# Performance work log

Hardware: AMD Instinct MI355X
Metric: run time of the kernel (lower is better)

## Reference

```python
import jax, jax.numpy as jnp
import numpy as np

D = 1024
H = 16
DH = D // H
MAX_TYPES = 256
B, L = 8, 1024
EPS = 1e-5


def setup_inputs() -> dict:
    key = jax.random.key(0)
    ks = jax.random.split(key, 16)
    s = 0.02
    return {
        'type_ids': jax.random.randint(ks[0], (B, L), 0, MAX_TYPES),
        'values': jax.random.normal(ks[1], (B, L, 1), jnp.float32),
        'deltas': jax.random.uniform(ks[2], (B, L, 1), jnp.float32),
        'type_emb': jax.random.normal(ks[3], (MAX_TYPES, D), jnp.float32) * s,
        'Wv': jax.random.normal(ks[4], (D, 1), jnp.float32) * s,
        'bv': jnp.zeros((D,), jnp.float32),
        'Wt': jax.random.normal(ks[5], (D, 1), jnp.float32) * s,
        'bt': jnp.zeros((D,), jnp.float32),
        'Win': jax.random.normal(ks[6], (3 * D, D), jnp.float32) * s,
        'bin': jnp.zeros((3 * D,), jnp.float32),
        'Wout': jax.random.normal(ks[7], (D, D), jnp.float32) * s,
        'bout': jnp.zeros((D,), jnp.float32),
        'W1': jax.random.normal(ks[8], (D, D), jnp.float32) * s,
        'b1': jnp.zeros((D,), jnp.float32),
        'W2': jax.random.normal(ks[9], (D, D), jnp.float32) * s,
        'b2': jnp.zeros((D,), jnp.float32),
        'gamma': jnp.ones((D,), jnp.float32),
        'beta': jnp.zeros((D,), jnp.float32),
    }


def _ln(x, gamma, beta):
    mu = jnp.mean(x, axis=-1, keepdims=True)
    var = jnp.mean(jnp.square(x - mu), axis=-1, keepdims=True)
    return (x - mu) * jax.lax.rsqrt(var + EPS) * gamma + beta


def reference(type_ids, values, deltas, type_emb, Wv, bv, Wt, bt,
              Win, bin, Wout, bout, W1, b1, W2, b2, gamma, beta):
    # fused embedding: type lookup + value/time linear projections
    h = type_emb[type_ids] + values @ Wv.T + bv + deltas @ Wt.T + bt  # [B,L,D]
    b, l, d = h.shape
    # multi-head self-attention (explicit weights path, need_weights=True)
    qkv = h @ Win.T + bin  # [B,L,3D]
    q, k, v = jnp.split(qkv, 3, axis=-1)
    q = q.reshape(b, l, H, DH)
    k = k.reshape(b, l, H, DH)
    v = v.reshape(b, l, H, DH)
    scale = 1.0 / jnp.sqrt(jnp.asarray(DH, h.dtype))
    scores = jnp.einsum('blhd,bmhd->bhlm', q, k) * scale  # [B,H,L,L]
    w = jax.nn.softmax(scores, axis=-1)
    attn = jnp.einsum('bhlm,bmhd->blhd', w, v).reshape(b, l, d)
    attn_out = attn @ Wout.T + bout
    h2 = _ln(h + attn_out, gamma, beta)
    ff = jax.nn.relu(h2 @ W1.T + b1) @ W2.T + b2
    h3 = _ln(h2 + ff, gamma, beta)
    pooled = h3.mean(axis=1)  # [B,D]
    attn_tokens = w.mean(axis=1).mean(axis=2)  # mean over heads, then keys -> [B,L]
    return pooled, attn_tokens
```

## Files before the change

kernel.cpp:

```cpp
#include <hip/hip_runtime.h>
#include <hip/hip_bf16.h>


#define Dm 1024
#define Hh 16
#define Bb 8
#define Ll 1024
#define Mm 8192
#define LNEPS 1e-5f

typedef __attribute__((ext_vector_type(8))) short s16x8;
typedef __attribute__((ext_vector_type(4))) short s16x4;
typedef __attribute__((ext_vector_type(4))) float f32x4;

using bf16 = __hip_bfloat16;

__device__ __forceinline__ short f2bs(float f) {
  return __builtin_bit_cast(short, __float2bfloat16(f));
}

__device__ __forceinline__ unsigned cvtpk(float lo, float hi) {
  unsigned r;
  asm("v_cvt_pk_bf16_f32 %0, %1, %2" : "=v"(r) : "v"(lo), "v"(hi));
  return r;
}

__device__ __forceinline__ void gload16(const void* g, void* l) {
  __builtin_amdgcn_global_load_lds(
      (__attribute__((address_space(1))) void*)g,
      (__attribute__((address_space(3))) void*)l, 16, 0, 0);
}

__global__ __launch_bounds__(256) void k_f2b(const float* __restrict__ x, bf16* __restrict__ y)
{
  const size_t i = ((size_t)blockIdx.x * 256 + threadIdx.x) * 4;
  const float4 v = *(const float4*)&x[i];
  s16x4 o;
  o[0] = f2bs(v.x); o[1] = f2bs(v.y); o[2] = f2bs(v.z); o[3] = f2bs(v.w);
  *(s16x4*)&y[i] = o;
}

__global__ __launch_bounds__(256) void k_embed(
    const int* __restrict__ tids, const float* __restrict__ vals, const float* __restrict__ dels,
    const float* __restrict__ temb, const float* __restrict__ Wv, const float* __restrict__ bv,
    const float* __restrict__ Wt, const float* __restrict__ bt,
    float* __restrict__ hf, bf16* __restrict__ hb)
{
  const int row = blockIdx.x;
  const int ty = tids[row];
  const float v = vals[row], dl = dels[row];
  const int d0 = threadIdx.x * 4;
  const float4 e  = *(const float4*)&temb[(size_t)ty * Dm + d0];
  const float4 wv = *(const float4*)&Wv[d0];
  const float4 c1 = *(const float4*)&bv[d0];
  const float4 wt = *(const float4*)&Wt[d0];
  const float4 c2 = *(const float4*)&bt[d0];
  float4 h;
  h.x = e.x + v * wv.x + c1.x + dl * wt.x + c2.x;
  h.y = e.y + v * wv.y + c1.y + dl * wt.y + c2.y;
  h.z = e.z + v * wv.z + c1.z + dl * wt.z + c2.z;
  h.w = e.w + v * wv.w + c1.w + dl * wt.w + c2.w;
  *(float4*)&hf[(size_t)row * Dm + d0] = h;
  s16x4 o;
  o[0] = f2bs(h.x); o[1] = f2bs(h.y); o[2] = f2bs(h.z); o[3] = f2bs(h.w);
  *(s16x4*)((short*)hb + (size_t)row * Dm + d0) = o;
}

template<bool RELU, bool OUTF, bool OUTB, bool RES>
__global__ __launch_bounds__(512) void k_gemm8(
    const bf16* __restrict__ A, const bf16* __restrict__ Bt,
    const float* __restrict__ bias, const float* __restrict__ res,
    float* __restrict__ outF, bf16* __restrict__ outB, const int N, const int K)
{
  __shared__ __attribute__((aligned(16))) short lds[49152];
  const int tid = threadIdx.x, lane = tid & 63, wave = tid >> 6;
  const int wr = wave >> 2, wc = wave & 3;
  const int l15 = lane & 15, lg = (lane >> 4) & 3;
  const int bm = blockIdx.x, bn = blockIdx.y;
  const int NT = K >> 6;

  const int rl = tid >> 3;
  const int swz = ((tid & 7) ^ (rl & 7)) * 8;
  const bf16* aSrc = A  + (size_t)(bm * 128 + rl) * K + swz;
  const bf16* bSrc = Bt + (size_t)(bn * 256 + rl) * K + swz;

  f32x4 acc[4][4] = {};

  auto stageA = [&](int t, int h) {
    gload16(aSrc + (size_t)h * 64 * K + t * 64,
            &lds[(t & 1) * 24576 + h * 4096 + tid * 8]);
  };
  auto stageB = [&](int t, int h) {
    gload16(bSrc + (size_t)h * 128 * K + t * 64,
            &lds[(t & 1) * 24576 + 8192 + h * 8192 + tid * 8]);
    gload16(bSrc + (size_t)(h * 128 + 64) * K + t * 64,
            &lds[(t & 1) * 24576 + 8192 + h * 8192 + 4096 + tid * 8]);
  };

  stageA(0, 0); stageA(0, 1); stageB(0, 0); stageB(0, 1);
  if (NT > 1) { stageA(1, 0); stageA(1, 1); }
  asm volatile("s_waitcnt vmcnt(2)" ::: "memory");
  __builtin_amdgcn_sched_barrier(0);
  __builtin_amdgcn_s_barrier();

  for (int t = 0; t < NT; ++t) {
    const int cb = (t & 1) * 24576;
    s16x8 fa[4][2], fb[2][2];

#pragma unroll
    for (int m = 0; m < 4; ++m)
#pragma unroll
      for (int ks = 0; ks < 2; ++ks) {
        const int row = wr * 64 + m * 16 + l15;
        fa[m][ks] = *(const s16x8*)&lds[cb + row * 64 + (((ks * 4 + lg) ^ (row & 7)) << 3)];
      }
#pragma unroll
    for (int n = 0; n < 2; ++n)
#pragma unroll
      for (int ks = 0; ks < 2; ++ks) {
        const int row = wc * 64 + n * 16 + l15;
        fb[n][ks] = *(const s16x8*)&lds[cb + 8192 + row * 64 + (((ks * 4 + lg) ^ (row & 7)) << 3)];
      }
    if (t + 1 < NT) { stageB(t + 1, 0); stageB(t + 1, 1); }
    __builtin_amdgcn_s_barrier();
    asm volatile("s_waitcnt lgkmcnt(0)" ::: "memory");
    __builtin_amdgcn_sched_barrier(0);
    __builtin_amdgcn_s_setprio(1);
#pragma unroll
    for (int m = 0; m < 4; ++m)
#pragma unroll
      for (int n = 0; n < 2; ++n)
#pragma unroll
        for (int ks = 0; ks < 2; ++ks)
          acc[m][n] = __builtin_amdgcn_mfma_f32_16x16x32_bf16(fa[m][ks], fb[n][ks], acc[m][n], 0, 0, 0);
    __builtin_amdgcn_s_setprio(0);
    __builtin_amdgcn_s_barrier();

#pragma unroll
    for (int n = 0; n < 2; ++n)
#pragma unroll
      for (int ks = 0; ks < 2; ++ks) {
        const int row = wc * 64 + (2 + n) * 16 + l15;
        fb[n][ks] = *(const s16x8*)&lds[cb + 8192 + row * 64 + (((ks * 4 + lg) ^ (row & 7)) << 3)];
      }
    if (t + 2 < NT) { stageA(t + 2, 0); stageA(t + 2, 1); }
    __builtin_amdgcn_s_barrier();
    asm volatile("s_waitcnt lgkmcnt(0)" ::: "memory");
    __builtin_amdgcn_sched_barrier(0);
    __builtin_amdgcn_s_setprio(1);
#pragma unroll
    for (int m = 0; m < 4; ++m)
#pragma unroll
      for (int n = 0; n < 2; ++n)
#pragma unroll
        for (int ks = 0; ks < 2; ++ks)
          acc[m][2 + n] = __builtin_amdgcn_mfma_f32_16x16x32_bf16(fa[m][ks], fb[n][ks], acc[m][2 + n], 0, 0, 0);
    __builtin_amdgcn_s_setprio(0);

    if (t + 1 < NT) {
      if (t + 2 < NT) asm volatile("s_waitcnt vmcnt(2)" ::: "memory");
      else            asm volatile("s_waitcnt vmcnt(0)" ::: "memory");
      __builtin_amdgcn_sched_barrier(0);
      __builtin_amdgcn_s_barrier();
    }
  }

#pragma unroll
  for (int n = 0; n < 4; ++n) {
    const int col = bn * 256 + wc * 64 + n * 16 + l15;
    const float bc = bias[col];
#pragma unroll
    for (int m = 0; m < 4; ++m) {
#pragma unroll
      for (int i = 0; i < 4; ++i) {
        const size_t row = (size_t)bm * 128 + wr * 64 + m * 16 + lg * 4 + i;
        float v = acc[m][n][i] + bc;
        if constexpr (RES)  v += res[row * N + col];
        if constexpr (RELU) v = fmaxf(v, 0.f);
        if constexpr (OUTF) outF[row * N + col] = v;
        if constexpr (OUTB) outB[row * N + col] = __float2bfloat16(v);
      }
    }
  }
}

__global__ __launch_bounds__(256) void k_vt(const bf16* __restrict__ qkv, bf16* __restrict__ vt)
{
  const int bh = blockIdx.x, lc = blockIdx.y;
  const int b = bh >> 4, h = bh & 15;
  __shared__ short tile[64][72];
  const int r = threadIdx.x >> 2;
  const int c0 = (threadIdx.x & 3) << 4;
  const short* src = (const short*)qkv + ((size_t)(b * Ll + lc * 64 + r)) * 3072 + 2048 + h * 64 + c0;
  const s16x8 x0 = *(const s16x8*)src;
  const s16x8 x1 = *(const s16x8*)(src + 8);
#pragma unroll
  for (int j = 0; j < 8; ++j) { tile[r][c0 + j] = x0[j]; tile[r][c0 + 8 + j] = x1[j]; }
  __syncthreads();
  s16x8 y0, y1;
#pragma unroll
  for (int j = 0; j < 8; ++j) { y0[j] = tile[c0 + j][r]; y1[j] = tile[c0 + 8 + j][r]; }
  short* dst = (short*)vt + ((size_t)(bh * 64 + r)) * Ll + lc * 64 + c0;
  *(s16x8*)dst = y0;
  *(s16x8*)(dst + 8) = y1;
}

__global__ __launch_bounds__(256) void k_attn(
    const bf16* __restrict__ qkv, const bf16* __restrict__ vt, bf16* __restrict__ attnb)
{
  const int bh = blockIdx.x;
  const int qb = blockIdx.y;
  const int b = bh >> 4, h = bh & 15;
  __shared__ __attribute__((aligned(16))) short lK[4096];
  __shared__ __attribute__((aligned(16))) short lV[4096];
  __shared__ __attribute__((aligned(16))) short lP[8192];
  const int tid = threadIdx.x, lane = tid & 63, wave = tid >> 6;
  const int l15 = lane & 15, lg = lane >> 4;
  const int qrow = wave * 32;
  const int l7 = l15 & 7;

  s16x8 qf[2][2];
#pragma unroll
  for (int mq = 0; mq < 2; ++mq)
#pragma unroll
    for (int ks = 0; ks < 2; ++ks)
      qf[mq][ks] = *(const s16x8*)((const short*)qkv +
          ((size_t)(b * Ll + qb * 128 + qrow + mq * 16 + l15)) * 3072 + h * 64 + ks * 32 + lg * 8);

  f32x4 o[2][4] = {};
  float rs[2] = {0.f, 0.f};

  const int sr = tid >> 3;
  const int swz = (tid & 7) ^ (sr & 7);

  for (int mc = 0; mc < 16; ++mc) {
    __syncthreads();
    {
      const bf16* gk = qkv + ((size_t)(b * Ll + mc * 64 + sr)) * 3072 + 1024 + h * 64 + swz * 8;
      gload16(gk,                     &lK[tid * 8]);
      gload16(gk + (size_t)32 * 3072, &lK[2048 + tid * 8]);
      const bf16* gv = vt + ((size_t)(bh * 64 + sr)) * Ll + mc * 64 + swz * 8;
      gload16(gv,                   &lV[tid * 8]);
      gload16(gv + (size_t)32 * Ll, &lV[2048 + tid * 8]);
    }
    __syncthreads();

    f32x4 st[2][4] = {};
    __builtin_amdgcn_s_setprio(1);
#pragma unroll
    for (int ks = 0; ks < 2; ++ks) {
#pragma unroll
      for (int n = 0; n < 4; ++n) {
        const int kr = n * 16 + l15;
        const s16x8 kf = *(const s16x8*)&lK[kr * 64 + (((ks * 4 + lg) ^ l7) << 3)];
        st[0][n] = __builtin_amdgcn_mfma_f32_16x16x32_bf16(kf, qf[0][ks], st[0][n], 0, 0, 0);
        st[1][n] = __builtin_amdgcn_mfma_f32_16x16x32_bf16(kf, qf[1][ks], st[1][n], 0, 0, 0);
      }
    }
    __builtin_amdgcn_s_setprio(0);

#pragma unroll
    for (int mq = 0; mq < 2; ++mq) {
      const int qr = qrow + mq * 16 + l15;
      short* prow = &lP[qr * 64];
      float loc = 0.f;
#pragma unroll
      for (int n = 0; n < 4; ++n) {
        const float e0 = __expf(st[mq][n][0] * 0.125f);
        const float e1 = __expf(st[mq][n][1] * 0.125f);
        const float e2 = __expf(st[mq][n][2] * 0.125f);
        const float e3 = __expf(st[mq][n][3] * 0.125f);
        loc += (e0 + e1) + (e2 + e3);
        const unsigned c0 = cvtpk(e0, e1);
        const unsigned c1 = cvtpk(e2, e3);
        const int col0 = n * 16 + lg * 4;
        const int scol = ((((col0 >> 3) ^ (qr & 7)) << 3) | (col0 & 7));
        *(unsigned*)&prow[scol]     = c0;
        *(unsigned*)&prow[scol + 2] = c1;
      }
      rs[mq] += loc;
    }

    __builtin_amdgcn_s_setprio(1);
#pragma unroll
    for (int ks = 0; ks < 2; ++ks) {
      s16x8 pa[2];
#pragma unroll
      for (int mq = 0; mq < 2; ++mq) {
        const int qr = qrow + mq * 16 + l15;
        pa[mq] = *(const s16x8*)&lP[qr * 64 + (((ks * 4 + lg) ^ (qr & 7)) << 3)];
      }
#pragma unroll
      for (int dn = 0; dn < 4; ++dn) {
        const int vr = dn * 16 + l15;
        const s16x8 vf = *(const s16x8*)&lV[vr * 64 + (((ks * 4 + lg) ^ l7) << 3)];
        o[0][dn] = __builtin_amdgcn_mfma_f32_16x16x32_bf16(pa[0], vf, o[0][dn], 0, 0, 0);
        o[1][dn] = __builtin_amdgcn_mfma_f32_16x16x32_bf16(pa[1], vf, o[1][dn], 0, 0, 0);
      }
    }
    __builtin_amdgcn_s_setprio(0);
  }

#pragma unroll
  for (int mq = 0; mq < 2; ++mq) {
    rs[mq] += __shfl_xor(rs[mq], 16);
    rs[mq] += __shfl_xor(rs[mq], 32);
  }
#pragma unroll
  for (int mq = 0; mq < 2; ++mq) {
    float inv[4];
#pragma unroll
    for (int i = 0; i < 4; ++i)
      inv[i] = 1.f / __shfl(rs[mq], lg * 4 + i);
#pragma unroll
    for (int dn = 0; dn < 4; ++dn) {
#pragma unroll
      for (int i = 0; i < 4; ++i) {
        const int q = qb * 128 + qrow + mq * 16 + lg * 4 + i;
        attnb[((size_t)(b * Ll + q)) * Dm + h * 64 + dn * 16 + l15] =
            __float2bfloat16(o[mq][dn][i] * inv[i]);
      }
    }
  }
}

template<bool WB>
__global__ __launch_bounds__(256) void k_ln(const float* __restrict__ x,
    const float* __restrict__ gamma, const float* __restrict__ beta,
    float* __restrict__ yf, bf16* __restrict__ yb)
{
  const size_t row = blockIdx.x;
  const int d0 = threadIdx.x * 4;
  const float4 xv = *(const float4*)&x[row * Dm + d0];
  float s  = xv.x + xv.y + xv.z + xv.w;
  float ss = xv.x * xv.x + xv.y * xv.y + xv.z * xv.z + xv.w * xv.w;
#pragma unroll
  for (int m = 1; m < 64; m <<= 1) { s += __shfl_xor(s, m); ss += __shfl_xor(ss, m); }
  __shared__ float red[8];
  const int wv = threadIdx.x >> 6;
  if ((threadIdx.x & 63) == 0) { red[wv] = s; red[4 + wv] = ss; }
  __syncthreads();
  s  = red[0] + red[1] + red[2] + red[3];
  ss = red[4] + red[5] + red[6] + red[7];
  const float mu = s * (1.f / Dm);
  const float rstd = rsqrtf(ss * (1.f / Dm) - mu * mu + LNEPS);
  const float4 g  = *(const float4*)&gamma[d0];
  const float4 be = *(const float4*)&beta[d0];
  float4 y;
  y.x = (xv.x - mu) * rstd * g.x + be.x;
  y.y = (xv.y - mu) * rstd * g.y + be.y;
  y.z = (xv.z - mu) * rstd * g.z + be.z;
  y.w = (xv.w - mu) * rstd * g.w + be.w;
  *(float4*)&yf[row * Dm + d0] = y;
  if constexpr (WB) {
    s16x4 o;
    o[0] = f2bs(y.x); o[1] = f2bs(y.y); o[2] = f2bs(y.z); o[3] = f2bs(y.w);
    *(s16x4*)((short*)yb + row * Dm + d0) = o;
  }
}

__global__ __launch_bounds__(256) void k_pool_part(const float* __restrict__ h3, float* __restrict__ part)
{
  const int b = blockIdx.x, lcn = blockIdx.y, dz = blockIdx.z;
  const int d = dz * 256 + threadIdx.x;
  float s = 0.f;
#pragma unroll 4
  for (int l = 0; l < 64; ++l)
    s += h3[((size_t)(b * Ll + lcn * 64 + l)) * Dm + d];
  part[((size_t)(b * 16 + lcn)) * Dm + d] = s;
}

__global__ __launch_bounds__(256) void k_pool_fin(const float* __restrict__ part, float* __restrict__ out)
{
  const int b = blockIdx.x;
  const int d = blockIdx.y * 256 + threadIdx.x;
  float s = 0.f;
#pragma unroll
  for (int c = 0; c < 16; ++c) s += part[((size_t)(b * 16 + c)) * Dm + d];
  out[b * Dm + d] = s * (1.f / Ll);
  out[(size_t)Mm + b * Dm + d] = 1.f / Ll;
}

extern "C" void kernel_launch(void* const* d_in, const int* in_sizes, int n_in,
                              void* d_out, int out_size, void* d_ws, size_t ws_size,
                              hipStream_t stream) {
  const int*   tids  = (const int*)  d_in[0];
  const float* vals  = (const float*)d_in[1];
  const float* dels  = (const float*)d_in[2];
  const float* temb  = (const float*)d_in[3];
  const float* Wv    = (const float*)d_in[4];
  const float* bv    = (const float*)d_in[5];
  const float* Wt    = (const float*)d_in[6];
  const float* bt    = (const float*)d_in[7];
  const float* Win   = (const float*)d_in[8];
  const float* bin   = (const float*)d_in[9];
  const float* Wout  = (const float*)d_in[10];
  const float* bout  = (const float*)d_in[11];
  const float* W1    = (const float*)d_in[12];
  const float* b1    = (const float*)d_in[13];
  const float* W2    = (const float*)d_in[14];
  const float* b2    = (const float*)d_in[15];
  const float* gamma = (const float*)d_in[16];
  const float* beta  = (const float*)d_in[17];
  float* out = (float*)d_out;

  char* w = (char*)d_ws;
  const size_t MB = 1ull << 20;
  float* hf    = (float*)(w + 0);
  bf16*  hb    = (bf16*) (w + 32 * MB);
  bf16*  qkv   = (bf16*) (w + 48 * MB);
  bf16*  vtb   = (bf16*) (w + 96 * MB);
  bf16*  attnb = (bf16*) (w + 112 * MB);
  float* x1    = (float*)(w + 48 * MB);
  float* h2f   = (float*)(w + 80 * MB);
  bf16*  h2b   = (bf16*) (w + 32 * MB);
  bf16*  ff1   = (bf16*) (w + 112 * MB);
  float* x2    = (float*)(w + 0);
  float* h3    = (float*)(w + 48 * MB);
  bf16*  WinB  = (bf16*) (w + 129 * MB);
  bf16*  WoutB = (bf16*) (w + 135 * MB);
  bf16*  W1B   = (bf16*) (w + 137 * MB);
  bf16*  W2B   = (bf16*) (w + 139 * MB);
  float* part  = (float*)(w + 141 * MB);

  k_f2b<<<3072, 256, 0, stream>>>(Win,  WinB);
  k_f2b<<<1024, 256, 0, stream>>>(Wout, WoutB);
  k_f2b<<<1024, 256, 0, stream>>>(W1,   W1B);
  k_f2b<<<1024, 256, 0, stream>>>(W2,   W2B);

  k_embed<<<Mm, 256, 0, stream>>>(tids, vals, dels, temb, Wv, bv, Wt, bt, hf, hb);

  k_gemm8<false, false, true, false><<<dim3(64, 12), 512, 0, stream>>>(
      hb, WinB, bin, nullptr, nullptr, qkv, 3072, 1024);

  k_vt<<<dim3(128, 16), 256, 0, stream>>>(qkv, vtb);
  k_attn<<<dim3(128, 8), 256, 0, stream>>>(qkv, vtb, attnb);

  k_gemm8<false, true, false, true><<<dim3(64, 4), 512, 0, stream>>>(
      attnb, WoutB, bout, hf, x1, nullptr, 1024, 1024);

  k_ln<true><<<Mm, 256, 0, stream>>>(x1, gamma, beta, h2f, h2b);

  k_gemm8<true, false, true, false><<<dim3(64, 4), 512, 0, stream>>>(
      h2b, W1B, b1, nullptr, nullptr, ff1, 1024, 1024);

  k_gemm8<false, true, false, true><<<dim3(64, 4), 512, 0, stream>>>(
      ff1, W2B, b2, h2f, x2, nullptr, 1024, 1024);

  k_ln<false><<<Mm, 256, 0, stream>>>(x2, gamma, beta, h3, nullptr);

  k_pool_part<<<dim3(8, 16, 4), 256, 0, stream>>>(h3, part);
  k_pool_fin<<<dim3(8, 4), 256, 0, stream>>>(part, out);
}
```

Baseline: 257.2 us.

## Triple-buffer B tiles in GEMM to prefetch two K-steps ahead

The bf16 GEMM kernel grows LDS from 96KB to 128KB and moves the B operand from double to triple buffering, so B tiles are prefetched two K-iterations ahead like A. The vmcnt waits are updated to allow six outstanding loads. The goal is to hide more global-load latency behind the MFMA work. In exchange, the larger LDS footprint can limit how many blocks fit per CU, and the buffer indexing becomes more complex.

Result: slower. 264.1 us (+2.7%).

```diff
diff --git a/kernel.cpp b/kernel.cpp
--- a/kernel.cpp
+++ b/kernel.cpp
@@ -72,7 +72,7 @@
     const float* __restrict__ bias, const float* __restrict__ res,
     float* __restrict__ outF, bf16* __restrict__ outB, const int N, const int K)
 {
-  __shared__ __attribute__((aligned(16))) short lds[49152];
+  __shared__ __attribute__((aligned(16))) short lds[65536];
   const int tid = threadIdx.x, lane = tid & 63, wave = tid >> 6;
   const int wr = wave >> 2, wc = wave & 3;
   const int l15 = lane & 15, lg = (lane >> 4) & 3;
@@ -86,25 +86,25 @@
 
   f32x4 acc[4][4] = {};
 
-  auto stageA = [&](int t, int h) {
-    gload16(aSrc + (size_t)h * 64 * K + t * 64,
-            &lds[(t & 1) * 24576 + h * 4096 + tid * 8]);
+  auto stageA = [&](int t) {
+    gload16(aSrc + t * 64,                   &lds[(t & 1) * 8192 + tid * 8]);
+    gload16(aSrc + (size_t)64 * K + t * 64,  &lds[(t & 1) * 8192 + 4096 + tid * 8]);
   };
   auto stageB = [&](int t, int h) {
-    gload16(bSrc + (size_t)h * 128 * K + t * 64,
-            &lds[(t & 1) * 24576 + 8192 + h * 8192 + tid * 8]);
-    gload16(bSrc + (size_t)(h * 128 + 64) * K + t * 64,
-            &lds[(t & 1) * 24576 + 8192 + h * 8192 + 4096 + tid * 8]);
+    const int boff = 16384 + (t % 3) * 16384 + h * 8192;
+    gload16(bSrc + (size_t)h * 128 * K + t * 64,        &lds[boff + tid * 8]);
+    gload16(bSrc + (size_t)(h * 128 + 64) * K + t * 64, &lds[boff + 4096 + tid * 8]);
   };
 
-  stageA(0, 0); stageA(0, 1); stageB(0, 0); stageB(0, 1);
-  if (NT > 1) { stageA(1, 0); stageA(1, 1); }
-  asm volatile("s_waitcnt vmcnt(2)" ::: "memory");
+  stageA(0); stageB(0, 0); stageB(0, 1);
+  if (NT > 1) { stageA(1); stageB(1, 0); stageB(1, 1); }
+  asm volatile("s_waitcnt vmcnt(6)" ::: "memory");
   __builtin_amdgcn_sched_barrier(0);
   __builtin_amdgcn_s_barrier();
 
   for (int t = 0; t < NT; ++t) {
-    const int cb = (t & 1) * 24576;
+    const int ca = (t & 1) * 8192;
+    const int cbB = 16384 + (t % 3) * 16384;
     s16x8 fa[4][2], fb[2][2];
 
 #pragma unroll
@@ -112,16 +112,16 @@
 #pragma unroll
       for (int ks = 0; ks < 2; ++ks) {
         const int row = wr * 64 + m * 16 + l15;
-        fa[m][ks] = *(const s16x8*)&lds[cb + row * 64 + (((ks * 4 + lg) ^ (row & 7)) << 3)];
+        fa[m][ks] = *(const s16x8*)&lds[ca + row * 64 + (((ks * 4 + lg) ^ (row & 7)) << 3)];
       }
 #pragma unroll
     for (int n = 0; n < 2; ++n)
 #pragma unroll
       for (int ks = 0; ks < 2; ++ks) {
         const int row = wc * 64 + n * 16 + l15;
-        fb[n][ks] = *(const s16x8*)&lds[cb + 8192 + row * 64 + (((ks * 4 + lg) ^ (row & 7)) << 3)];
-      }
-    if (t + 1 < NT) { stageB(t + 1, 0); stageB(t + 1, 1); }
+        fb[n][ks] = *(const s16x8*)&lds[cbB + row * 64 + (((ks * 4 + lg) ^ (row & 7)) << 3)];
+      }
+    if (t + 2 < NT) stageB(t + 2, 0);
     __builtin_amdgcn_s_barrier();
     asm volatile("s_waitcnt lgkmcnt(0)" ::: "memory");
     __builtin_amdgcn_sched_barrier(0);
@@ -141,9 +141,9 @@
 #pragma unroll
       for (int ks = 0; ks < 2; ++ks) {
         const int row = wc * 64 + (2 + n) * 16 + l15;
-        fb[n][ks] = *(const s16x8*)&lds[cb + 8192 + row * 64 + (((ks * 4 + lg) ^ (row & 7)) << 3)];
-      }
-    if (t + 2 < NT) { stageA(t + 2, 0); stageA(t + 2, 1); }
+        fb[n][ks] = *(const s16x8*)&lds[cbB + row * 64 + (((ks * 4 + lg) ^ (row & 7)) << 3)];
+      }
+    if (t + 2 < NT) { stageB(t + 2, 1); stageA(t + 2); }
     __builtin_amdgcn_s_barrier();
     asm volatile("s_waitcnt lgkmcnt(0)" ::: "memory");
     __builtin_amdgcn_sched_barrier(0);
@@ -158,7 +158,7 @@
     __builtin_amdgcn_s_setprio(0);
 
     if (t + 1 < NT) {
-      if (t + 2 < NT) asm volatile("s_waitcnt vmcnt(2)" ::: "memory");
+      if (t + 2 < NT) asm volatile("s_waitcnt vmcnt(6)" ::: "memory");
       else            asm volatile("s_waitcnt vmcnt(0)" ::: "memory");
       __builtin_amdgcn_sched_barrier(0);
       __builtin_amdgcn_s_barrier();
```
